# Kernel optimization log

Measured on AMD Instinct MI355X. Metric: run time of the kernel, lower is better.

Reference implementation:

```python
import jax, jax.numpy as jnp
import numpy as np
from jax import lax

MB = 8          # block_size (macroblock)
P = 8           # search_distance
CROP = 17       # space_crop
TAU = 1         # causal delay
LARGE = 65537.0 # sentinel cost (matches skvideo DS)
MAX_STEPS = 16  # LDSP step cap (|displacement| <= P, each step moves >=1)

# Large / Small Diamond Search Patterns, entries are (dx, dy)
LDSP = jnp.array([[0, -2], [-1, -1], [1, -1], [-2, 0], [0, 0], [2, 0], [-1, 1], [1, 1], [0, 2]], dtype=jnp.int32)
SDSP = jnp.array([[0, -1], [-1, 0], [0, 0], [1, 0], [0, 1]], dtype=jnp.int32)


def _ds_motion_frame(imgP, imgI):
    """Diamond-search block motion of current frame imgP w.r.t. reference imgI.
    Returns (nbr, nbc, 2) int32 motion vectors (dy, dx)."""
    H, W = imgP.shape
    nbr, nbc = H // MB, W // MB
    # (nbr, nbc, MB, MB) macroblocks of the current frame
    blocks = imgP.reshape(nbr, MB, nbc, MB).transpose(0, 2, 1, 3)
    bi = jnp.arange(nbr, dtype=jnp.int32) * MB
    bj = jnp.arange(nbc, dtype=jnp.int32) * MB

    def cost_at(blk, i, j, y, x):
        # MAD cost of matching blk (at block origin i,j) against imgI at (y,x);
        # out-of-image or outside the +/-P search window -> LARGE.
        valid = ((y >= 0) & (y + MB <= H) & (x >= 0) & (x + MB <= W)
                 & (jnp.abs(y - i) <= P) & (jnp.abs(x - j) <= P))
        yc = jnp.clip(y, 0, H - MB)
        xc = jnp.clip(x, 0, W - MB)
        ref = lax.dynamic_slice(imgI, (yc, xc), (MB, MB))
        return jnp.where(valid, jnp.mean(jnp.abs(blk - ref)), LARGE)

    def ds_one(blk, i, j):
        c0 = cost_at(blk, i, j, i, j)
        # skvideo: if center cost is exactly 0, skip the LDSP stage
        init_pt = jnp.where(c0 == 0.0, 4, -1).astype(jnp.int32)

        def cond(st):
            return (st[2] != 4) & (st[3] < MAX_STEPS)

        def body(st):
            y, x, _, k = st
            costs = jax.vmap(lambda d: cost_at(blk, i, j, y + d[1], x + d[0]))(LDSP)
            pt = jnp.argmin(costs).astype(jnp.int32)
            return (y + LDSP[pt, 1], x + LDSP[pt, 0], pt, k + 1)

        y, x, _, _ = lax.while_loop(cond, body, (i, j, init_pt, jnp.int32(0)))
        # final small-diamond refinement
        sc = jax.vmap(lambda d: cost_at(blk, i, j, y + d[1], x + d[0]))(SDSP)
        spt = jnp.argmin(sc).astype(jnp.int32)
        y = y + SDSP[spt, 1]
        x = x + SDSP[spt, 0]
        return jnp.stack([y - i, x - j])  # (dy, dx)

    row = jax.vmap(lambda blkrow, i: jax.vmap(lambda blk, j: ds_one(blk, i, j))(blkrow, bj))
    return row(blocks, bi)


def _block_comp_frame(ref, motion):
    """Motion-compensate one frame from reference `ref` using per-block (dy,dx)."""
    nbr, nbc = motion.shape[:2]
    bi = jnp.arange(nbr, dtype=jnp.int32) * MB
    bj = jnp.arange(nbc, dtype=jnp.int32) * MB

    def get(i, j, m):
        return lax.dynamic_slice(ref, (i + m[0], j + m[1]), (MB, MB))

    blocks = jax.vmap(lambda i, mrow: jax.vmap(lambda j, m: get(i, j, m))(bj, mrow))(bi, motion)
    return blocks.transpose(0, 2, 1, 3).reshape(nbr * MB, nbc * MB)


def _predict_video(vid):
    """vid: (T, H, W). Causal branch: motion between (t-1, t) warps frame t to predict t+1."""
    vid_sg = lax.stop_gradient(vid)  # motion vectors are integer-valued, non-differentiable
    motion = jax.vmap(_ds_motion_frame)(vid_sg[1:], vid_sg[:-1])  # (T-1, nbr, nbc, 2)
    v = vid[TAU:]  # blockComp(videodata[tau:], motion[:-tau])
    comp_rest = jax.vmap(_block_comp_frame)(v[:-1], motion[:-TAU])
    comp = jnp.concatenate([v[:1], comp_rest], axis=0)  # comp[0] = first frame copy
    target = v[1:, CROP:-CROP, CROP:-CROP]
    pred = comp[1:, CROP:-CROP, CROP:-CROP]
    return target, pred


def setup_inputs() -> dict:
    key = jax.random.key(0)
    x = jax.random.normal(key, (4, 1, 16, 512, 512), dtype=jnp.float32)
    return {"x": x}


def reference(x):
    vids = x[:, 0]  # single (luminance) channel, (B, T, H, W)
    target, pred = jax.vmap(_predict_video)(vids)
    # restore channel dim: (B, 1, T-2, H-2c, W-2c)
    return target[:, None], pred[:, None]
```

## Files before the change

kernel.cpp:

```cpp
#include <hip/hip_runtime.h>

#define HH 512
#define WW 512
#define TT 16
#define NF 14
#define NV 4
#define CRP 17
#define CW 478
#define TGT_SIZE ((size_t)NV * NF * CW * CW)
#define FRAME ((size_t)HH * WW)

#define WROWS 48
#define WCOLS 80
#define WSTR  84
#define CPY   (WROWS * WSTR)
#define TH    1e-3f

__device__ __forceinline__ float bf8_sum(float v) {
    v += __shfl_xor(v, 1, 64);
    v += __shfl_xor(v, 2, 64);
    v += __shfl_xor(v, 4, 64);
    return v;
}
__device__ __forceinline__ double bf8_sumd(double v) {
    v += __shfl_xor(v, 1, 64);
    v += __shfl_xor(v, 2, 64);
    v += __shfl_xor(v, 4, 64);
    return v;
}

__device__ __forceinline__ float sad_f32(const float* bp, const float2* pr2) {
    const float2* w2 = (const float2*)bp;
    float2 a0 = w2[0], a1 = w2[1], a2 = w2[2], a3 = w2[3];
    float t0 = fabsf(pr2[0].x - a0.x) + fabsf(pr2[0].y - a0.y);
    float t1 = fabsf(pr2[1].x - a1.x) + fabsf(pr2[1].y - a1.y);
    float t2 = fabsf(pr2[2].x - a2.x) + fabsf(pr2[2].y - a2.y);
    float t3 = fabsf(pr2[3].x - a3.x) + fabsf(pr2[3].y - a3.y);
    return bf8_sum((t0 + t1) + (t2 + t3));
}

__device__ __forceinline__ double sad_f64(const float* bp, const float2* pr2) {
    const float2* w2 = (const float2*)bp;
    float2 a0 = w2[0], a1 = w2[1], a2 = w2[2], a3 = w2[3];
    double e0 = (double)fabsf(pr2[0].x - a0.x) + (double)fabsf(pr2[0].y - a0.y);
    double e1 = (double)fabsf(pr2[1].x - a1.x) + (double)fabsf(pr2[1].y - a1.y);
    double e2 = (double)fabsf(pr2[2].x - a2.x) + (double)fabsf(pr2[2].y - a2.y);
    double e3 = (double)fabsf(pr2[3].x - a3.x) + (double)fabsf(pr2[3].y - a3.y);
    return bf8_sumd((e0 + e1) + (e2 + e3));
}

__global__ void __launch_bounds__(256)
motion_pred_kernel(const float* __restrict__ x, float* __restrict__ out) {
    __shared__ float win[2 * CPY];

    int cta = blockIdx.x;
    int jb0 = (cta & 7) * 64;
    int bi0 = ((cta >> 3) & 15) * 4;
    int bf  = cta >> 7;
    int f   = bf % NF;
    int b   = bf / NF;

    const float* imgP = x + (size_t)(b * TT + f + 1) * FRAME;
    const float* imgI = x + (size_t)(b * TT + f)     * FRAME;

    int wy0 = bi0 * 8 - 8;
    int wx0 = jb0 - 8;

    #pragma unroll
    for (int t = 0; t < 4; ++t) {
        int idx = t * 256 + threadIdx.x;
        if (idx < WROWS * (WCOLS / 4)) {
            int row = idx / (WCOLS / 4);
            int c4  = idx - row * (WCOLS / 4);
            int yy  = wy0 + row;
            int xg  = wx0 + c4 * 4;
            if (yy >= 0 && yy < HH && xg >= 0 && xg <= WW - 4) {
                float4 v = *(const float4*)(imgI + (size_t)yy * WW + xg);
                *(float4*)(win + row * WSTR + c4 * 4) = v;
                const float* vv = &v.x;
                #pragma unroll
                for (int k2 = 0; k2 < 4; ++k2) {
                    int oo = c4 * 4 + k2 - 1;
                    if (oo >= 0) win[CPY + row * WSTR + oo] = vv[k2];
                }
            }
        }
    }
    __syncthreads();

    int w    = threadIdx.x >> 6;
    int lane = threadIdx.x & 63;
    int g = lane >> 3;
    int r = lane & 7;

    int i  = (bi0 + w) * 8;
    int jg = jb0 + g * 8;

    float2 pr2[4];
    {
        const float4* prow = (const float4*)(imgP + (size_t)(i + r) * WW + jg);
        float4 p0 = prow[0], p1 = prow[1];
        pr2[0] = make_float2(p0.x, p0.y); pr2[1] = make_float2(p0.z, p0.w);
        pr2[2] = make_float2(p1.x, p1.y); pr2[3] = make_float2(p1.z, p1.w);
    }

    int y = i, xx = jg;
    const float* A0; const float* A1;
    bool vy[5], vx[5];

    auto precomp = [&]() {
        int o = xx - wx0;
        int p = o & 1;
        int rowoff = (y - wy0 + r) * WSTR;
        A0 = win + (p ? CPY : 0) + rowoff + (o - p);
        A1 = win + (p ? 0 : CPY) + rowoff + (o - (1 - p));
        int dyL = y - i, dxL = xx - jg;
        int ylo = max(-8 - dyL, -y), yhi = min(8 - dyL, (HH - 8) - y);
        int xlo = max(-8 - dxL, -xx), xhi = min(8 - dxL, (WW - 8) - xx);
        #pragma unroll
        for (int d = -2; d <= 2; ++d) {
            vy[d + 2] = (d >= ylo) && (d <= yhi);
            vx[d + 2] = (d >= xlo) && (d <= xhi);
        }
    };
    auto evalq = [&](int dy, int dx) -> float {
        const float* bp = ((dx & 1) ? A1 : A0) + (dy * WSTR + dx);
        float s = sad_f32(bp, pr2);
        return (vy[dy + 2] && vx[dx + 2]) ? s : 1e30f;
    };
    auto evalqd = [&](int dy, int dx) -> double {
        const float* bp = ((dx & 1) ? A1 : A0) + (dy * WSTR + dx);
        double s = sad_f64(bp, pr2);
        return (vy[dy + 2] && vx[dx + 2]) ? s : 1e30;
    };

    const int LDx[9] = {0,-1, 1,-2, 0, 2,-1, 1, 0};
    const int LDy[9] = {-2,-1,-1, 0, 0, 0, 1, 1, 2};

    precomp();
    float cc = sad_f32(A0, pr2);
    bool done = (cc == 0.0f);
    int k = 0;

    while (__any((!done) && (k < 16))) {
        bool active = (!done) && (k < 16);
        precomp();
        float cf[9];
        float m1 = 1e38f, m2 = 1e38f; int b1 = 0;
        #pragma unroll
        for (int q = 0; q < 9; ++q) {
            float cq = (q == 4) ? cc : evalq(LDy[q], LDx[q]);
            cf[q] = cq;
            bool lt = cq < m1;
            m2 = lt ? m1 : fminf(m2, cq);
            m1 = lt ? cq : m1;
            b1 = lt ? q  : b1;
        }
        bool needx = (m2 - m1) < TH;
        if (__any(active && needx)) {
            double e1 = 1e300; int eb = 0;
            #pragma unroll
            for (int q = 0; q < 9; ++q) {
                double eq = evalqd(LDy[q], LDx[q]);
                bool lt = eq < e1;
                e1 = lt ? eq : e1; eb = lt ? q : eb;
            }
            float mf = cf[0];
            #pragma unroll
            for (int q = 1; q < 9; ++q) mf = (eb == q) ? cf[q] : mf;
            if (needx) { b1 = eb; m1 = mf; }
        }
        if (active) {
            int dy = (b1 == 0) ? -2 : (b1 == 1 || b1 == 2) ? -1
                   : (b1 == 6 || b1 == 7) ? 1 : (b1 == 8) ? 2 : 0;
            int dx = (b1 == 1 || b1 == 6) ? -1 : (b1 == 2 || b1 == 7) ? 1
                   : (b1 == 3) ? -2 : (b1 == 5) ? 2 : 0;
            y += dy; xx += dx;
            cc = m1;
            done = (b1 == 4);
            k++;
        }
    }

    {
        precomp();
        const int SDx[5] = {0,-1, 0, 1, 0};
        const int SDy[5] = {-1, 0, 0, 0, 1};
        float m1 = 1e38f, m2 = 1e38f; int sb = 0;
        #pragma unroll
        for (int q = 0; q < 5; ++q) {
            float cq = (q == 2) ? cc : evalq(SDy[q], SDx[q]);
            bool lt = cq < m1;
            m2 = lt ? m1 : fminf(m2, cq);
            m1 = lt ? cq : m1;
            sb = lt ? q  : sb;
        }
        bool needx = (m2 - m1) < TH;
        if (__any(needx)) {
            double e1 = 1e300; int eb = 0;
            #pragma unroll
            for (int q = 0; q < 5; ++q) {
                double eq = evalqd(SDy[q], SDx[q]);
                bool lt = eq < e1;
                e1 = lt ? eq : e1; eb = lt ? q : eb;
            }
            if (needx) sb = eb;
        }
        y  += (sb == 0) ? -1 : (sb == 4) ? 1 : 0;
        xx += (sb == 1) ? -1 : (sb == 3) ? 1 : 0;
    }

    int dy = y - i, dx = xx - jg;

    int gy = i + r;
    if (gy >= CRP && gy < HH - CRP) {
        const float* src = imgP + (size_t)(i + dy + r) * WW + (jg + dx);
        size_t obase = TGT_SIZE
            + (((size_t)(b * NF + f)) * CW + (size_t)(gy - CRP)) * CW - CRP;
        #pragma unroll
        for (int c = 0; c < 8; ++c) {
            int gx = jg + c;
            if (gx >= CRP && gx < WW - CRP)
                out[obase + gx] = src[c];
        }
    }
}

__global__ void __launch_bounds__(256)
target_copy_kernel(const float* __restrict__ x, float* __restrict__ out) {
    unsigned idx = blockIdx.x * 256 + threadIdx.x;
    if (idx >= (unsigned)(TGT_SIZE / 4)) return;
    unsigned o = idx * 4;
    unsigned fidx = o / (CW * CW);
    unsigned rem  = o - fidx * (CW * CW);
    unsigned rr   = rem / CW;
    unsigned c0   = rem - rr * CW;
    unsigned b    = fidx / NF, fi = fidx - b * NF;
    const float* src = x + (size_t)(b * TT + fi + 2) * FRAME;
    float4 v;
    float* vp = &v.x;
    #pragma unroll
    for (int t = 0; t < 4; ++t) {
        unsigned cc2 = c0 + t, r2 = rr;
        if (cc2 >= CW) { cc2 -= CW; r2 += 1; }
        vp[t] = src[(r2 + CRP) * WW + cc2 + CRP];
    }
    *(float4*)(out + o) = v;
}

extern "C" void kernel_launch(void* const* d_in, const int* in_sizes, int n_in,
                              void* d_out, int out_size, void* d_ws, size_t ws_size,
                              hipStream_t stream) {
    const float* x = (const float*)d_in[0];
    float* out = (float*)d_out;

    {
        int n4 = (int)(TGT_SIZE / 4);
        int blocks = (n4 + 255) / 256;
        target_copy_kernel<<<blocks, 256, 0, stream>>>(x, out);
    }
    {
        int blocks = NV * NF * 16 * 8;
        motion_pred_kernel<<<blocks, 256, 0, stream>>>(x, out);
    }
}
```

Baseline: 250.0 us.

## Share LDS window loads across diamond points and use DPP reductions

Each diamond search step now loads one row segment per dy offset (with extra float2s) into registers and reuses overlapping pairs across the points at the same row, instead of doing four separate LDS loads per candidate. The 8-lane float reduction replaces __shfl_xor with DPP row permutes, which avoids ds_bpermute traffic. Validity bounds are precomputed once per block. The cost is higher register pressure from holding the loaded segments.

Result: faster. 233.5 us (-6.6%).

```diff
diff --git a/kernel.cpp b/kernel.cpp
--- a/kernel.cpp
+++ b/kernel.cpp
@@ -16,10 +16,15 @@
 #define CPY   (WROWS * WSTR)
 #define TH    1e-3f
 
+template <int CTRL>
+__device__ __forceinline__ float dpp_add(float v) {
+    int x = __builtin_amdgcn_update_dpp(0, __float_as_int(v), CTRL, 0xF, 0xF, true);
+    return v + __int_as_float(x);
+}
 __device__ __forceinline__ float bf8_sum(float v) {
-    v += __shfl_xor(v, 1, 64);
-    v += __shfl_xor(v, 2, 64);
-    v += __shfl_xor(v, 4, 64);
+    v = dpp_add<0xB1>(v);
+    v = dpp_add<0x4E>(v);
+    v = dpp_add<0x141>(v);
     return v;
 }
 __device__ __forceinline__ double bf8_sumd(double v) {
@@ -29,9 +34,8 @@
     return v;
 }
 
-__device__ __forceinline__ float sad_f32(const float* bp, const float2* pr2) {
-    const float2* w2 = (const float2*)bp;
-    float2 a0 = w2[0], a1 = w2[1], a2 = w2[2], a3 = w2[3];
+__device__ __forceinline__ float sad4(float2 a0, float2 a1, float2 a2, float2 a3,
+                                      const float2* pr2) {
     float t0 = fabsf(pr2[0].x - a0.x) + fabsf(pr2[0].y - a0.y);
     float t1 = fabsf(pr2[1].x - a1.x) + fabsf(pr2[1].y - a1.y);
     float t2 = fabsf(pr2[2].x - a2.x) + fabsf(pr2[2].y - a2.y);
@@ -104,6 +108,9 @@
         pr2[2] = make_float2(p1.x, p1.y); pr2[3] = make_float2(p1.z, p1.w);
     }
 
+    int yLo = max(i - 8, 0),  yHi = min(i + 8, HH - 8);
+    int xLo = max(jg - 8, 0), xHi = min(jg + 8, WW - 8);
+
     int y = i, xx = jg;
     const float* A0; const float* A1;
     bool vy[5], vx[5];
@@ -114,19 +121,11 @@
         int rowoff = (y - wy0 + r) * WSTR;
         A0 = win + (p ? CPY : 0) + rowoff + (o - p);
         A1 = win + (p ? 0 : CPY) + rowoff + (o - (1 - p));
-        int dyL = y - i, dxL = xx - jg;
-        int ylo = max(-8 - dyL, -y), yhi = min(8 - dyL, (HH - 8) - y);
-        int xlo = max(-8 - dxL, -xx), xhi = min(8 - dxL, (WW - 8) - xx);
         #pragma unroll
         for (int d = -2; d <= 2; ++d) {
-            vy[d + 2] = (d >= ylo) && (d <= yhi);
-            vx[d + 2] = (d >= xlo) && (d <= xhi);
-        }
-    };
-    auto evalq = [&](int dy, int dx) -> float {
-        const float* bp = ((dx & 1) ? A1 : A0) + (dy * WSTR + dx);
-        float s = sad_f32(bp, pr2);
-        return (vy[dy + 2] && vx[dx + 2]) ? s : 1e30f;
+            vy[d + 2] = (y + d >= yLo) && (y + d <= yHi);
+            vx[d + 2] = (xx + d >= xLo) && (xx + d <= xHi);
+        }
     };
     auto evalqd = [&](int dy, int dx) -> double {
         const float* bp = ((dx & 1) ? A1 : A0) + (dy * WSTR + dx);
@@ -138,19 +137,60 @@
     const int LDy[9] = {-2,-1,-1, 0, 0, 0, 1, 1, 2};
 
     precomp();
-    float cc = sad_f32(A0, pr2);
+    float cc;
+    {
+        const float2* a0 = (const float2*)A0;
+        float2 c0 = a0[0], c1 = a0[1], c2 = a0[2], c3 = a0[3];
+        cc = sad4(c0, c1, c2, c3, pr2);
+    }
     bool done = (cc == 0.0f);
     int k = 0;
 
     while (__any((!done) && (k < 16))) {
         bool active = (!done) && (k < 16);
         precomp();
+
+        const float2* am2 = (const float2*)(A0 - 2 * WSTR);
+        const float2* am1 = (const float2*)(A1 - WSTR - 1);
+        const float2* az  = (const float2*)(A0 - 2);
+        const float2* ap1 = (const float2*)(A1 + WSTR - 1);
+        const float2* ap2 = (const float2*)(A0 + 2 * WSTR);
+        float2 wm2[4], wm1[5], wz[6], wp1[5], wp2[4];
+        #pragma unroll
+        for (int t = 0; t < 4; ++t) wm2[t] = am2[t];
+        #pragma unroll
+        for (int t = 0; t < 5; ++t) wm1[t] = am1[t];
+        #pragma unroll
+        for (int t = 0; t < 6; ++t) wz[t]  = az[t];
+        #pragma unroll
+        for (int t = 0; t < 5; ++t) wp1[t] = ap1[t];
+        #pragma unroll
+        for (int t = 0; t < 4; ++t) wp2[t] = ap2[t];
+
+        float s0 = sad4(wm2[0], wm2[1], wm2[2], wm2[3], pr2);
+        float s1 = sad4(wm1[0], wm1[1], wm1[2], wm1[3], pr2);
+        float s2 = sad4(wm1[1], wm1[2], wm1[3], wm1[4], pr2);
+        float s3 = sad4(wz[0],  wz[1],  wz[2],  wz[3],  pr2);
+        float s5 = sad4(wz[2],  wz[3],  wz[4],  wz[5],  pr2);
+        float s6 = sad4(wp1[0], wp1[1], wp1[2], wp1[3], pr2);
+        float s7 = sad4(wp1[1], wp1[2], wp1[3], wp1[4], pr2);
+        float s8 = sad4(wp2[0], wp2[1], wp2[2], wp2[3], pr2);
+
         float cf[9];
+        cf[0] = (vy[0] && vx[2]) ? s0 : 1e30f;
+        cf[1] = (vy[1] && vx[1]) ? s1 : 1e30f;
+        cf[2] = (vy[1] && vx[3]) ? s2 : 1e30f;
+        cf[3] = (vy[2] && vx[0]) ? s3 : 1e30f;
+        cf[4] = cc;
+        cf[5] = (vy[2] && vx[4]) ? s5 : 1e30f;
+        cf[6] = (vy[3] && vx[1]) ? s6 : 1e30f;
+        cf[7] = (vy[3] && vx[3]) ? s7 : 1e30f;
+        cf[8] = (vy[4] && vx[2]) ? s8 : 1e30f;
+
         float m1 = 1e38f, m2 = 1e38f; int b1 = 0;
         #pragma unroll
         for (int q = 0; q < 9; ++q) {
-            float cq = (q == 4) ? cc : evalq(LDy[q], LDx[q]);
-            cf[q] = cq;
+            float cq = cf[q];
             bool lt = cq < m1;
             m2 = lt ? m1 : fminf(m2, cq);
             m1 = lt ? cq : m1;
@@ -186,10 +226,34 @@
         precomp();
         const int SDx[5] = {0,-1, 0, 1, 0};
         const int SDy[5] = {-1, 0, 0, 0, 1};
+
+        const float2* sm1 = (const float2*)(A0 - WSTR);
+        const float2* sz  = (const float2*)(A1 - 1);
+        const float2* sp1 = (const float2*)(A0 + WSTR);
+        float2 um1[4], uz[5], up1[4];
+        #pragma unroll
+        for (int t = 0; t < 4; ++t) um1[t] = sm1[t];
+        #pragma unroll
+        for (int t = 0; t < 5; ++t) uz[t]  = sz[t];
+        #pragma unroll
+        for (int t = 0; t < 4; ++t) up1[t] = sp1[t];
+
+        float t0 = sad4(um1[0], um1[1], um1[2], um1[3], pr2);
+        float t1 = sad4(uz[0],  uz[1],  uz[2],  uz[3],  pr2);
+        float t3 = sad4(uz[1],  uz[2],  uz[3],  uz[4],  pr2);
+        float t4 = sad4(up1[0], up1[1], up1[2], up1[3], pr2);
+
+        float cf5[5];
+        cf5[0] = (vy[1] && vx[2]) ? t0 : 1e30f;
+        cf5[1] = (vy[2] && vx[1]) ? t1 : 1e30f;
+        cf5[2] = cc;
+        cf5[3] = (vy[2] && vx[3]) ? t3 : 1e30f;
+        cf5[4] = (vy[3] && vx[2]) ? t4 : 1e30f;
+
         float m1 = 1e38f, m2 = 1e38f; int sb = 0;
         #pragma unroll
         for (int q = 0; q < 5; ++q) {
-            float cq = (q == 2) ? cc : evalq(SDy[q], SDx[q]);
+            float cq = cf5[q];
             bool lt = cq < m1;
             m2 = lt ? m1 : fminf(m2, cq);
             m1 = lt ? cq : m1;
```
